# Kernel optimization log

Hardware: AMD Instinct MI355X
Metric: run time of the kernel (lower is better)

## Reference

```python
import jax, jax.numpy as jnp
import numpy as np
import math

N = 100000
E = 1600000
D_IN = 128
H = 128
OUT = 10
NEG = -1e30


def setup_inputs() -> dict:
    key = jax.random.key(0)
    ks = jax.random.split(key, 24)
    def lin(k, fi, fo):
        s = 1.0 / np.sqrt(fi)
        return jax.random.uniform(k, (fi, fo), jnp.float32, -s, s)
    inp = {
        'x': jax.random.normal(ks[0], (N, D_IN), jnp.float32),
        'edge_index': jax.random.randint(ks[1], (2, E), 0, N, jnp.int64),
        'W1': lin(ks[2], D_IN, H), 'b1': jnp.zeros((H,), jnp.float32),
        'ws1': lin(ks[3], H, 1), 'bs1': jnp.zeros((1,), jnp.float32),
        'W2': lin(ks[4], H, H), 'b2': jnp.zeros((H,), jnp.float32),
        'ws2': lin(ks[5], H, 1), 'bs2': jnp.zeros((1,), jnp.float32),
        'W3': lin(ks[6], H, H), 'b3': jnp.zeros((H,), jnp.float32),
        'ws3': lin(ks[7], H, 1), 'bs3': jnp.zeros((1,), jnp.float32),
        'M1': lin(ks[8], 2 * H, H), 'bm1': jnp.zeros((H,), jnp.float32),
        'M2': lin(ks[9], H, H // 2), 'bm2': jnp.zeros((H // 2,), jnp.float32),
        'M3': lin(ks[10], H // 2, OUT), 'bm3': jnp.zeros((OUT,), jnp.float32),
    }
    return inp


def _gcn(x, W, b, src, dst, node_mask, edge_mask):
    # GCNConv with self-loops: deg[i] = self_loop + in_degree over valid edges
    deg = node_mask + jax.ops.segment_sum(edge_mask, dst, num_segments=N)
    dinv = jnp.where(deg > 0, jax.lax.rsqrt(deg), 0.0)
    coef = edge_mask * dinv[src] * dinv[dst]            # [E]
    agg = jax.ops.segment_sum(coef[:, None] * x[src], dst, num_segments=N)
    agg = agg + (node_mask * dinv * dinv)[:, None] * x   # self-loop term
    return (agg @ W + b) * node_mask[:, None]


def _sag_pool(x, ws, bs, src, dst, node_mask, edge_mask, k):
    # score via 1-dim GCNConv, top-k (ratio 0.5) select, tanh gating, edge filtering
    score = _gcn(x, ws, bs, src, dst, node_mask, edge_mask)[:, 0]
    _, idx = jax.lax.top_k(jnp.where(node_mask > 0, score, -jnp.inf), k)
    new_mask = jnp.zeros((N,), x.dtype).at[idx].set(1.0)
    x_new = x * jnp.tanh(score)[:, None] * new_mask[:, None]
    e_new = edge_mask * new_mask[src] * new_mask[dst]
    return x_new, new_mask, e_new


def _readout(x, mask, k):
    mean = jnp.sum(x * mask[:, None], axis=0) / k
    mx = jnp.max(jnp.where(mask[:, None] > 0, x, NEG), axis=0)
    return jnp.concatenate([mean, mx])[None, :]   # [1, 2H]


def reference(x, edge_index, W1, b1, ws1, bs1, W2, b2, ws2, bs2, W3, b3, ws3, bs3, M1, bm1, M2, bm2, M3, bm3):
    src, dst = edge_index[0], edge_index[1]
    nm0 = jnp.ones((N,), jnp.float32)
    em0 = jnp.ones((E,), jnp.float32)
    k1 = math.ceil(0.5 * N)
    k2 = math.ceil(0.5 * k1)
    k3 = math.ceil(0.5 * k2)

    h1 = jax.nn.relu(_gcn(x, W1, b1, src, dst, nm0, em0))
    x1, nm1, em1 = _sag_pool(h1, ws1, bs1, src, dst, nm0, em0, k1)
    r1 = _readout(x1, nm1, k1)

    h2 = jax.nn.relu(_gcn(x1, W2, b2, src, dst, nm1, em1))
    x2, nm2, em2 = _sag_pool(h2, ws2, bs2, src, dst, nm1, em1, k2)
    r2 = _readout(x2, nm2, k2)

    h3 = jax.nn.relu(_gcn(x2, W3, b3, src, dst, nm2, em2))
    x3, nm3, em3 = _sag_pool(h3, ws3, bs3, src, dst, nm2, em2, k3)
    r3 = _readout(x3, nm3, k3)

    readout = r1 + r2 + r3                              # [1, 2H]
    y = jax.nn.relu(readout @ M1 + bm1)
    y = jax.nn.relu(y @ M2 + bm2)
    y = y @ M3 + bm3
    return jax.nn.log_softmax(y, axis=1)
```

## Files before the change

### kernel.cpp

```cpp
#include <hip/hip_runtime.h>
#include <cstdint>
#include <cstddef>

#define NN 100000
#define EE 1600000
#define HH 128
#define NB_N 391
#define NBKT 391
#define CAP 5120
#define NCH 16
#define SPC 25


typedef float f32x2 __attribute__((ext_vector_type(2)));
typedef float f32x4 __attribute__((ext_vector_type(4)));
typedef short bf16x8 __attribute__((ext_vector_type(8)));

static __device__ __forceinline__ unsigned fsort_(float f){
  unsigned u = __float_as_uint(f);
  return (u & 0x80000000u) ? ~u : (u | 0x80000000u);
}
static __device__ __forceinline__ unsigned bfbits_(float f){
  unsigned u = __float_as_uint(f);
  return (u + 0x7FFFu + ((u >> 16) & 1u)) >> 16;
}
static __device__ __forceinline__ unsigned bfpack_(float f0, float f1){
  return bfbits_(f0) | (bfbits_(f1) << 16);
}
static __device__ __forceinline__ float bflo_(unsigned u){ return __uint_as_float(u << 16); }
static __device__ __forceinline__ float bfhi_(unsigned u){ return __uint_as_float(u & 0xFFFF0000u); }

__global__ void k_init(const int* __restrict__ ei, unsigned* __restrict__ state,
                       unsigned* __restrict__ bktcnt,
                       const float* __restrict__ W0, const float* __restrict__ W1,
                       const float* __restrict__ W2,
                       unsigned short* __restrict__ WtH, unsigned short* __restrict__ WtL){
  int t = threadIdx.x;
  if(blockIdx.x == 3){
    if(t < 64){
      int v = ei[2*t + 1];
      unsigned long long m = __ballot(v != 0);
      if(t == 0) state[8] = (m == 0ull) ? 1u : 0u;
    }
    if(t >= 12 && t < 24) state[t] = 0u;
    for(int j=t; j<NBKT; j+=256) bktcnt[j] = 0u;
  } else {
    int m = blockIdx.x;
    const float* W = (m==0)?W0:((m==1)?W1:W2);
    unsigned short* th = WtH + m*16384;
    unsigned short* tl = WtL + m*16384;
    for(int i=t; i<16384; i+=256){
      int k = i & 127, n = i >> 7;
      float w = W[k*128 + n];
      unsigned hb = bfbits_(w);
      float hf = __uint_as_float(hb<<16);
      unsigned lb = bfbits_(w - hf);
      th[n*128 + k] = (unsigned short)hb;
      tl[n*128 + k] = (unsigned short)lb;
    }
  }
}

__global__ __launch_bounds__(256) void k_binA(const int* __restrict__ ei,
                     const unsigned* __restrict__ state,
                     unsigned* __restrict__ bktcnt, unsigned* __restrict__ staging){
  __shared__ unsigned lcnt[NBKT];
  __shared__ unsigned gbase[NBKT];
  __shared__ unsigned lloc[NBKT];
  __shared__ unsigned pfx[512];
  __shared__ unsigned sortv[4096];
  __shared__ unsigned short bktid[4096];
  int t = threadIdx.x;
  for(int j=t; j<NBKT; j+=256){ lcnt[j] = 0u; lloc[j] = 0u; }
  bool i64 = (state[8] != 0u);
  int e0 = blockIdx.x*4096;
  int es[16], ed[16];
  #pragma unroll
  for(int k=0;k<16;k++){
    int e = e0 + k*256 + t;
    int s = -1, d = 0;
    if(e < EE){
      if(i64){ s = ei[2*e]; d = ei[2*EE + 2*e]; }
      else   { s = ei[e];   d = ei[EE + e]; }
    }
    es[k] = s; ed[k] = d;
  }
  __syncthreads();
  #pragma unroll
  for(int k=0;k<16;k++){
    if(es[k] >= 0) atomicAdd(&lcnt[ed[k]>>8], 1u);
  }
  __syncthreads();
  int j0 = t, j1 = t + 256;
  pfx[j0] = (j0 < NBKT) ? lcnt[j0] : 0u;
  pfx[j1] = (j1 < NBKT) ? lcnt[j1] : 0u;
  __syncthreads();
  for(int off=1; off<512; off<<=1){
    unsigned u0 = (j0 >= off) ? pfx[j0-off] : 0u;
    unsigned u1 = (j1 >= off) ? pfx[j1-off] : 0u;
    __syncthreads();
    pfx[j0] += u0;
    pfx[j1] += u1;
    __syncthreads();
  }
  unsigned total = pfx[NBKT-1];
  for(int j=t; j<NBKT; j+=256){
    unsigned c = lcnt[j];
    gbase[j] = c ? atomicAdd(&bktcnt[j], c) : 0u;
  }
  __syncthreads();
  #pragma unroll
  for(int k=0;k<16;k++){
    if(es[k] >= 0){
      int b = ed[k] >> 8;
      unsigned slot = (pfx[b] - lcnt[b]) + atomicAdd(&lloc[b], 1u);
      sortv[slot] = (unsigned)es[k] | (((unsigned)(ed[k] & 255)) << 17);
      bktid[slot] = (unsigned short)b;
    }
  }
  __syncthreads();
  for(unsigned i=t; i<total; i+=256){
    unsigned b = bktid[i];
    unsigned local = i - (pfx[b] - lcnt[b]);
    unsigned off = gbase[b] + local;
    if(off < CAP) staging[b*CAP + off] = sortv[i];
  }
}

__global__ __launch_bounds__(256) void k_binB(const unsigned* __restrict__ staging,
                     const unsigned* __restrict__ bktcnt,
                     int* __restrict__ rs, int* __restrict__ rl, int* __restrict__ col,
                     float* __restrict__ dinv){
  __shared__ unsigned hist[256];
  __shared__ unsigned pref[256];
  __shared__ unsigned lfill[256];
  __shared__ unsigned baseSh;
  __shared__ int colsh[CAP];
  int t = threadIdx.x;
  int b = blockIdx.x;
  unsigned s = 0;
  for(int j=t; j<b; j+=256) s += bktcnt[j];
  pref[t] = s;
  __syncthreads();
  for(int off=128; off>0; off>>=1){
    if(t < off) pref[t] += pref[t+off];
    __syncthreads();
  }
  if(t == 0) baseSh = pref[0];
  __syncthreads();
  unsigned base = baseSh;
  unsigned cnt = bktcnt[b]; if(cnt > CAP) cnt = CAP;
  hist[t] = 0u; lfill[t] = 0u;
  __syncthreads();
  const unsigned* st = staging + (unsigned)b*CAP;
  for(unsigned i=t; i<cnt; i+=256) atomicAdd(&hist[st[i]>>17], 1u);
  __syncthreads();
  unsigned h = hist[t];
  pref[t] = h;
  __syncthreads();
  for(int off=1; off<256; off<<=1){
    unsigned u = (t >= off) ? pref[t-off] : 0u;
    __syncthreads();
    pref[t] += u;
    __syncthreads();
  }
  unsigned excl = pref[t] - h;
  int node = b*256 + t;
  if(node < NN){
    rs[node] = (int)(base + excl);
    rl[node] = (int)h;
    dinv[node] = rsqrtf(1.f + (float)h);
  }
  __syncthreads();
  pref[t] = excl;
  __syncthreads();
  for(unsigned i=t; i<cnt; i+=256){
    unsigned w = st[i];
    unsigned dl = w >> 17;
    unsigned pos = pref[dl] + atomicAdd(&lfill[dl], 1u);
    colsh[pos] = (int)(w & 0x1FFFFu);
  }
  __syncthreads();
  for(unsigned i=t; i<cnt; i+=256) col[base+i] = colsh[i];
}

template<int MODE>
__global__ __launch_bounds__(256) void k_gemmM(const void* __restrict__ xin_,
        const float* __restrict__ gate, const float* __restrict__ dinv,
        const int* __restrict__ alist, int nrows,
        const unsigned short* __restrict__ WtH, const unsigned short* __restrict__ WtL,
        unsigned short* __restrict__ y16){
  __shared__ __attribute__((aligned(16))) unsigned short sWh[128*128];
  __shared__ __attribute__((aligned(16))) unsigned short sWl[128*128];
  __shared__ __attribute__((aligned(16))) unsigned short sB[4][16*128];
  int t = threadIdx.x;
  for(int f = t; f < 2048; f += 256){
    int colw = f >> 4, kc = f & 15;
    uint4 vh = *(const uint4*)(WtH + colw*128 + kc*8);
    uint4 vl = *(const uint4*)(WtL + colw*128 + kc*8);
    int dst = colw*128 + ((kc ^ (colw & 15)) << 3);
    *(uint4*)&sWh[dst] = vh;
    *(uint4*)&sWl[dst] = vl;
  }
  int lane = t & 63, wid = t >> 6;
  int lg = lane >> 4, lc = lane & 15;
  int rb = blockIdx.x*64 + wid*16;
  int arow = rb + lc;
  int anode = 0;
  if(arow < nrows) anode = MODE ? alist[arow] : arow;
  bf16x8 a_h[4], a_l[4];
  if(MODE){
    const unsigned short* xp = (const unsigned short*)xin_ + (size_t)anode*HH + lg*8;
    #pragma unroll
    for(int kw=0;kw<4;kw++) a_h[kw] = *(const bf16x8*)(xp + kw*32);
  } else {
    const float* xp = (const float*)xin_ + (size_t)anode*HH + lg*8;
    #pragma unroll
    for(int kw=0;kw<4;kw++){
      float4 x0 = *(const float4*)(xp + kw*32);
      float4 x1 = *(const float4*)(xp + kw*32 + 4);
      float xs[8] = {x0.x,x0.y,x0.z,x0.w,x1.x,x1.y,x1.z,x1.w};
      #pragma unroll
      for(int e=0;e<8;e++){
        unsigned hb = bfbits_(xs[e]);
        float hf = __uint_as_float(hb<<16);
        unsigned lb = bfbits_(xs[e]-hf);
        a_h[kw][e] = (short)hb;
        a_l[kw][e] = (short)lb;
      }
    }
  }
  __syncthreads();
  f32x4 acc[8];
  #pragma unroll
  for(int c=0;c<8;c++) acc[c] = (f32x4){0.f,0.f,0.f,0.f};
  #pragma unroll
  for(int kw=0;kw<4;kw++){
    int kch = kw*4 + lg;
    bf16x8 bh[8], bl[8];
    #pragma unroll
    for(int c=0;c<8;c++){
      int idx = (c*16 + lc)*128 + ((kch ^ lc) << 3);
      bh[c] = *(const bf16x8*)&sWh[idx];
      bl[c] = *(const bf16x8*)&sWl[idx];
    }
    #pragma unroll
    for(int c=0;c<8;c++)
      acc[c] = __builtin_amdgcn_mfma_f32_16x16x32_bf16(a_h[kw], bh[c], acc[c], 0,0,0);
    if(MODE){
      #pragma unroll
      for(int c=0;c<8;c++)
        acc[c] = __builtin_amdgcn_mfma_f32_16x16x32_bf16(a_h[kw], bl[c], acc[c], 0,0,0);
    } else {
      #pragma unroll
      for(int c=0;c<8;c++)
        acc[c] = __builtin_amdgcn_mfma_f32_16x16x32_bf16(a_l[kw], bh[c], acc[c], 0,0,0);
      #pragma unroll
      for(int c=0;c<8;c++)
        acc[c] = __builtin_amdgcn_mfma_f32_16x16x32_bf16(a_h[kw], bl[c], acc[c], 0,0,0);
    }
  }
  float s[4];
  #pragma unroll
  for(int r=0;r<4;r++){
    int gr = rb + lg*4 + r;
    float sv = 0.f;
    if(gr < nrows){
      int nd = MODE ? alist[gr] : gr;
      sv = MODE ? dinv[nd]*gate[nd] : dinv[nd];
    }
    s[r] = sv;
  }
  #pragma unroll
  for(int c=0;c<8;c++){
    #pragma unroll
    for(int r=0;r<4;r++)
      sB[wid][(lg*4+r)*128 + c*16 + lc] = (unsigned short)bfbits_(acc[c][r]*s[r]);
  }
  #pragma unroll
  for(int it=0; it<4; it++){
    int row = it*4 + lg;
    int grow = rb + row;
    uint4 v = *(const uint4*)&sB[wid][row*128 + lc*8];
    if(grow < nrows){
      int nd = MODE ? alist[grow] : grow;
      *(uint4*)&y16[(size_t)nd*HH + lc*8] = v;
    }
  }
}

#define ACCQ(V) do{ \
  f32x2 t0,t1,t2,t3; \
  t0.x=__uint_as_float((V).x<<16); t0.y=__uint_as_float((V).x&0xFFFF0000u); \
  t1.x=__uint_as_float((V).y<<16); t1.y=__uint_as_float((V).y&0xFFFF0000u); \
  t2.x=__uint_as_float((V).z<<16); t2.y=__uint_as_float((V).z&0xFFFF0000u); \
  t3.x=__uint_as_float((V).w<<16); t3.y=__uint_as_float((V).w&0xFFFF0000u); \
  a01+=t0; a23+=t1; a45+=t2; a67+=t3; }while(0)

template<int LIST>
__global__ __launch_bounds__(256) void k_agg(const unsigned short* __restrict__ y16,
        const float* __restrict__ dinv,
        const int* __restrict__ rs, const int* __restrict__ rl,
        const int* __restrict__ col, const int* __restrict__ alist,
        const float* __restrict__ bias, const float* __restrict__ wsc,
        unsigned short* __restrict__ h16, float* __restrict__ p,
        unsigned* __restrict__ hist){
  if(blockIdx.x < 512) hist[blockIdx.x*256 + threadIdx.x] = 0u;
  int w = (blockIdx.x*256 + threadIdx.x) >> 6;
  int lane = threadIdx.x & 63;
  int g = lane >> 4, c = lane & 15;
  int node = LIST ? alist[w] : w;
  float di = dinv[node];
  int e0 = rs[node], len = rl[node];
  const char* yb = (const char*)y16;
  unsigned lc16 = (unsigned)(c << 4);
  int chunk = (len + 3) >> 2;
  int ib = g*chunk;
  int ie = ib + chunk; if(ie > len) ie = len;
  f32x2 a01 = {0.f,0.f}, a23 = {0.f,0.f}, a45 = {0.f,0.f}, a67 = {0.f,0.f};
  const int* ce = col + e0;
  int i = ib;
  for(; i+3 < ie; i += 4){
    int c0 = ce[i], c1 = ce[i+1], c2 = ce[i+2], c3 = ce[i+3];
    uint4 v0 = *(const uint4*)(yb + (((unsigned)c0<<8) | lc16));
    uint4 v1 = *(const uint4*)(yb + (((unsigned)c1<<8) | lc16));
    uint4 v2 = *(const uint4*)(yb + (((unsigned)c2<<8) | lc16));
    uint4 v3 = *(const uint4*)(yb + (((unsigned)c3<<8) | lc16));
    ACCQ(v0); ACCQ(v1); ACCQ(v2); ACCQ(v3);
  }
  for(; i < ie; i++){
    int c0 = ce[i];
    uint4 v0 = *(const uint4*)(yb + (((unsigned)c0<<8) | lc16));
    ACCQ(v0);
  }
  float a0=a01.x, a1=a01.y, a2=a23.x, a3=a23.y, a4=a45.x, a5=a45.y, a6=a67.x, a7=a67.y;
  a0 += __shfl_xor(a0,16,64); a0 += __shfl_xor(a0,32,64);
  a1 += __shfl_xor(a1,16,64); a1 += __shfl_xor(a1,32,64);
  a2 += __shfl_xor(a2,16,64); a2 += __shfl_xor(a2,32,64);
  a3 += __shfl_xor(a3,16,64); a3 += __shfl_xor(a3,32,64);
  a4 += __shfl_xor(a4,16,64); a4 += __shfl_xor(a4,32,64);
  a5 += __shfl_xor(a5,16,64); a5 += __shfl_xor(a5,32,64);
  a6 += __shfl_xor(a6,16,64); a6 += __shfl_xor(a6,32,64);
  a7 += __shfl_xor(a7,16,64); a7 += __shfl_xor(a7,32,64);
  uint4 sv = *(const uint4*)(yb + (((unsigned)node<<8) | lc16));
  const float4* b4 = (const float4*)bias;
  float4 bb0 = b4[2*c], bb1 = b4[2*c+1];
  float o0 = fmaxf(fmaf(di, a0 + bflo_(sv.x), bb0.x), 0.f);
  float o1 = fmaxf(fmaf(di, a1 + bfhi_(sv.x), bb0.y), 0.f);
  float o2 = fmaxf(fmaf(di, a2 + bflo_(sv.y), bb0.z), 0.f);
  float o3 = fmaxf(fmaf(di, a3 + bfhi_(sv.y), bb0.w), 0.f);
  float o4 = fmaxf(fmaf(di, a4 + bflo_(sv.z), bb1.x), 0.f);
  float o5 = fmaxf(fmaf(di, a5 + bfhi_(sv.z), bb1.y), 0.f);
  float o6 = fmaxf(fmaf(di, a6 + bflo_(sv.w), bb1.z), 0.f);
  float o7 = fmaxf(fmaf(di, a7 + bfhi_(sv.w), bb1.w), 0.f);
  if(g == 0){
    uint4 o;
    o.x = bfpack_(o0,o1); o.y = bfpack_(o2,o3);
    o.z = bfpack_(o4,o5); o.w = bfpack_(o6,o7);
    ((uint4*)(h16 + (size_t)node*HH))[c] = o;
  }
  const float4* w4 = (const float4*)wsc;
  float4 w0 = w4[2*c], w1 = w4[2*c+1];
  float pp = o0*w0.x + o1*w0.y + o2*w0.z + o3*w0.w
           + o4*w1.x + o5*w1.y + o6*w1.z + o7*w1.w;
  pp += __shfl_xor(pp, 1, 64);
  pp += __shfl_xor(pp, 2, 64);
  pp += __shfl_xor(pp, 4, 64);
  pp += __shfl_xor(pp, 8, 64);
  if(lane == 0) p[node] = di*pp;
}

template<int LIST>
__global__ void k_score(const float* __restrict__ p, const float* __restrict__ dinv,
                        const int* __restrict__ rs, const int* __restrict__ rl,
                        const int* __restrict__ col, const int* __restrict__ alist, int n,
                        const float* __restrict__ bs, float* __restrict__ score,
                        unsigned* __restrict__ key, unsigned* __restrict__ hist){
  int w = blockIdx.x*256 + threadIdx.x;
  if(w >= n) return;
  int i = LIST ? alist[w] : w;
  float di = dinv[i];
  float s = 0.f;
  int e0 = rs[i], len = rl[i];
  const int* ce = col + e0;
  int e = 0;
  for(; e+3 < len; e += 4){
    int c0 = ce[e], c1 = ce[e+1], c2 = ce[e+2], c3 = ce[e+3];
    s += (p[c0] + p[c1]) + (p[c2] + p[c3]);
  }
  for(; e < len; e++) s += p[ce[e]];
  float sc = di*(s + p[i]) + bs[0];
  score[i] = sc;
  unsigned kv = fsort_(sc);
  key[i] = kv;
  atomicAdd(&hist[kv>>16], 1u);
}

__global__ void k_hist_lo(const unsigned* __restrict__ key, const unsigned* __restrict__ state,
                          unsigned* __restrict__ histB){
  int i = blockIdx.x*256 + threadIdx.x;
  if(i < NN){
    unsigned kv = key[i];
    if((kv >> 16) == state[0]) atomicAdd(&histB[kv & 0xFFFFu], 1u);
  }
}
__global__ void k_pick(const unsigned* __restrict__ hist, unsigned* __restrict__ state,
                       int k_in, int mode){
  __shared__ unsigned csum[256];
  __shared__ unsigned vrow[256];
  __shared__ int rowSh;
  __shared__ unsigned aboveSh;
  int t = threadIdx.x;
  const uint4* h4 = (const uint4*)(hist + t*256);
  unsigned s = 0;
  for(int j=0;j<64;j++){ uint4 v = h4[j]; s += v.x+v.y+v.z+v.w; }
  csum[t] = s;
  if(t == 0) rowSh = -1;
  __syncthreads();
  for(int off=1; off<256; off<<=1){
    unsigned v = (t+off < 256) ? csum[t+off] : 0u;
    __syncthreads();
    csum[t] += v;
    __syncthreads();
  }
  unsigned k = (mode == 0) ? (unsigned)k_in : state[1];
  unsigned above = csum[t] - s;
  if(above < k && above + s >= k){ rowSh = t; aboveSh = above; }
  __syncthreads();
  int row = rowSh;
  if(row >= 0){
    vrow[t] = hist[row*256 + t];
    __syncthreads();
    for(int off=1; off<256; off<<=1){
      unsigned u = (t+off < 256) ? vrow[t+off] : 0u;
      __syncthreads();
      vrow[t] += u;
      __syncthreads();
    }
    unsigned above2 = aboveSh;
    unsigned sincl = vrow[t];
    unsigned snext = (t < 255) ? vrow[t+1] : 0u;
    bool cond  = (above2 + sincl >= k);
    bool condn = (above2 + snext >= k);
    if(cond && !condn){
      unsigned run = above2 + snext;
      if(mode == 0){ state[0] = (unsigned)(row*256+t); state[1] = k - run; }
      else { state[2] = (state[0] << 16) | (unsigned)(row*256+t); state[3] = k - run; }
    }
  }
}

__global__ __launch_bounds__(256) void k_maskCR(unsigned* __restrict__ key,
        const float* __restrict__ score, const unsigned* __restrict__ state,
        const unsigned short* __restrict__ h16,
        unsigned* __restrict__ selb, float* __restrict__ gate,
        int* __restrict__ alist_out, unsigned* __restrict__ acounter,
        float* __restrict__ rpart, int slotbase){
  __shared__ int wcnt[4];
  __shared__ int priorSh;
  __shared__ int redi[256];
  __shared__ float gl[256];
  __shared__ unsigned char slf[256];
  __shared__ float4 red[256];
  __shared__ float out2[256];
  int t = threadIdx.x;
  int i = blockIdx.x*256 + t;
  unsigned T = state[2];
  int trem = (int)state[3];
  unsigned kv = (i < NN) ? key[i] : 0u;
  bool match = (kv == T);
  unsigned long long m = __ballot(match);
  int lane = t & 63, wid = t >> 6;
  if(lane == 0) wcnt[wid] = __popcll(m);
  if(t == 0) priorSh = 0;
  __syncthreads();
  int hasMatch = wcnt[0] | wcnt[1] | wcnt[2] | wcnt[3];
  int bbase = blockIdx.x*256;
  if(hasMatch){
    int cm = 0;
    for(int j = t*4; j < bbase; j += 1024){
      uint4 kk = *(const uint4*)&key[j];
      cm += (kk.x==T) + (kk.y==T) + (kk.z==T) + (kk.w==T);
    }
    redi[t] = cm;
    __syncthreads();
    for(int off=128; off>0; off>>=1){
      if(t < off) redi[t] += redi[t+off];
      __syncthreads();
    }
    if(t == 0) priorSh = redi[0];
    __syncthreads();
  }
  int pre = 0;
  for(int w=0; w<wid; w++) pre += wcnt[w];
  int lrank = __popcll(m & ((1ull << lane) - 1ull));
  int rank = priorSh + pre + lrank;
  bool sel = (kv > T) || (match && rank < trem);
  float gg = sel ? tanhf(score[i]) : 0.f;
  gl[t] = gg;
  slf[t] = sel ? 1 : 0;
  if(i < NN){
    gate[i] = gg;
    if(!sel) key[i] = 0u;
  }
  unsigned long long sm = __ballot(sel);
  if(lane == 0){
    int widx = blockIdx.x*4 + wid;
    selb[widx*2]   = (unsigned)sm;
    selb[widx*2+1] = (unsigned)(sm >> 32);
  }
  unsigned abase = 0;
  if(lane == 0) abase = atomicAdd(acounter, (unsigned)__popcll(sm));
  abase = (unsigned)__shfl((int)abase, 0, 64);
  if(sel) alist_out[abase + __popcll(sm & ((1ull << lane) - 1ull))] = i;
  __syncthreads();
  int ch = t & 15;
  int slot = t >> 4;
  float mm[8] = {0,0,0,0,0,0,0,0};
  float MM[8] = {-1e30f,-1e30f,-1e30f,-1e30f,-1e30f,-1e30f,-1e30f,-1e30f};
  for(int itr=0; itr<16; itr++){
    int nl = slot + itr*16;
    int node = bbase + nl;
    if(node < NN && slf[nl]){
      float g = gl[nl];
      uint4 v = ((const uint4*)(h16 + (size_t)node*HH))[ch];
      float x0 = g*bflo_(v.x), x1 = g*bfhi_(v.x);
      float x2 = g*bflo_(v.y), x3 = g*bfhi_(v.y);
      float x4 = g*bflo_(v.z), x5 = g*bfhi_(v.z);
      float x6 = g*bflo_(v.w), x7 = g*bfhi_(v.w);
      mm[0]+=x0; mm[1]+=x1; mm[2]+=x2; mm[3]+=x3;
      mm[4]+=x4; mm[5]+=x5; mm[6]+=x6; mm[7]+=x7;
      MM[0]=fmaxf(MM[0],x0); MM[1]=fmaxf(MM[1],x1); MM[2]=fmaxf(MM[2],x2); MM[3]=fmaxf(MM[3],x3);
      MM[4]=fmaxf(MM[4],x4); MM[5]=fmaxf(MM[5],x5); MM[6]=fmaxf(MM[6],x6); MM[7]=fmaxf(MM[7],x7);
    }
  }
  #pragma unroll
  for(int half=0; half<2; half++){
    red[t] = make_float4(mm[half*4+0],mm[half*4+1],mm[half*4+2],mm[half*4+3]);
    __syncthreads();
    if(t < 16){
      float4 sacc = red[t];
      for(int j=1;j<16;j++){
        float4 o = red[t + 16*j];
        sacc.x += o.x; sacc.y += o.y; sacc.z += o.z; sacc.w += o.w;
      }
      int d = t*8 + half*4;
      out2[d+0] = sacc.x; out2[d+1] = sacc.y; out2[d+2] = sacc.z; out2[d+3] = sacc.w;
    }
    __syncthreads();
    red[t] = make_float4(MM[half*4+0],MM[half*4+1],MM[half*4+2],MM[half*4+3]);
    __syncthreads();
    if(t < 16){
      float4 sacc = red[t];
      for(int j=1;j<16;j++){
        float4 o = red[t + 16*j];
        sacc.x = fmaxf(sacc.x,o.x); sacc.y = fmaxf(sacc.y,o.y);
        sacc.z = fmaxf(sacc.z,o.z); sacc.w = fmaxf(sacc.w,o.w);
      }
      int d = 128 + t*8 + half*4;
      out2[d+0] = sacc.x; out2[d+1] = sacc.y; out2[d+2] = sacc.z; out2[d+3] = sacc.w;
    }
    __syncthreads();
  }
  rpart[(size_t)(slotbase + blockIdx.x)*256 + t] = out2[t];
}

__global__ __launch_bounds__(256) void k_compact(const int* __restrict__ alist, int n,
        const unsigned* __restrict__ selb,
        const int* __restrict__ rs_old, const int* __restrict__ rl_old,
        const int* __restrict__ col_old,
        int* __restrict__ rs_new, int* __restrict__ rl_new, int* __restrict__ col_new,
        float* __restrict__ dinv, unsigned* __restrict__ ecnt){
  __shared__ unsigned gcnt[16];
  __shared__ unsigned gbase[16];
  __shared__ unsigned blkbase;
  int t = threadIdx.x;
  int g = t >> 4, lane = t & 15;
  int gsh = ((t >> 4) & 3) * 16;
  int idx = blockIdx.x*16 + g;
  int node = -1, e0 = 0, len = 0;
  if(idx < n){ node = alist[idx]; e0 = rs_old[node]; len = rl_old[node]; }
  int cnt = 0;
  for(int i=lane; i<len; i+=16){
    int s = col_old[e0+i];
    cnt += (int)((selb[s>>5] >> (s&31)) & 1u);
  }
  cnt += __shfl_xor(cnt,1,64); cnt += __shfl_xor(cnt,2,64);
  cnt += __shfl_xor(cnt,4,64); cnt += __shfl_xor(cnt,8,64);
  if(lane == 0) gcnt[g] = (node >= 0) ? (unsigned)cnt : 0u;
  __syncthreads();
  if(t == 0){
    unsigned s = 0;
    for(int j=0;j<16;j++){ gbase[j] = s; s += gcnt[j]; }
    blkbase = s ? atomicAdd(ecnt, s) : 0u;
  }
  __syncthreads();
  unsigned base = blkbase + gbase[g];
  if(node >= 0 && lane == 0){
    rs_new[node] = (int)base;
    rl_new[node] = cnt;
    dinv[node] = rsqrtf(1.f + (float)cnt);
  }
  int pos = (int)base;
  for(int i0=0; i0<len; i0+=16){
    int i = i0 + lane;
    bool keep = false; int s = 0;
    if(i < len){ s = col_old[e0+i]; keep = ((selb[s>>5] >> (s&31)) & 1u) != 0u; }
    unsigned long long b = __ballot(keep);
    unsigned gb = (unsigned)((b >> gsh) & 0xFFFFull);
    int rank = __popc(gb & ((1u << lane) - 1u));
    if(keep) col_new[pos + rank] = s;
    pos += __popc(gb);
  }
}

__global__ void k_red(const float* __restrict__ rpart, float* __restrict__ rpart2){
  int l = blockIdx.x >> 4, c = blockIdx.x & 15;
  int t = threadIdx.x;
  int j0 = c*SPC, j1 = j0 + SPC; if(j1 > NB_N) j1 = NB_N;
  const float* rp = rpart + (size_t)l*NB_N*256;
  float r;
  if(t < 128){
    float s0=0.f,s1=0.f,s2=0.f,s3=0.f;
    int j = j0;
    for(; j+3 < j1; j += 4){
      s0 += rp[(size_t)(j  )*256 + t];
      s1 += rp[(size_t)(j+1)*256 + t];
      s2 += rp[(size_t)(j+2)*256 + t];
      s3 += rp[(size_t)(j+3)*256 + t];
    }
    for(; j < j1; j++) s0 += rp[(size_t)j*256 + t];
    r = (s0+s1)+(s2+s3);
  } else {
    float m0=-1e30f,m1=-1e30f,m2=-1e30f,m3=-1e30f;
    int j = j0;
    for(; j+3 < j1; j += 4){
      m0 = fmaxf(m0, rp[(size_t)(j  )*256 + t]);
      m1 = fmaxf(m1, rp[(size_t)(j+1)*256 + t]);
      m2 = fmaxf(m2, rp[(size_t)(j+2)*256 + t]);
      m3 = fmaxf(m3, rp[(size_t)(j+3)*256 + t]);
    }
    for(; j < j1; j++) m0 = fmaxf(m0, rp[(size_t)j*256 + t]);
    r = fmaxf(fmaxf(m0,m1), fmaxf(m2,m3));
  }
  rpart2[(size_t)blockIdx.x*256 + t] = r;
}

__global__ void k_mlp(const float* __restrict__ rpart2,
                      const float* __restrict__ M1, const float* __restrict__ bm1,
                      const float* __restrict__ M2, const float* __restrict__ bm2,
                      const float* __restrict__ M3, const float* __restrict__ bm3,
                      float* __restrict__ out){
  __shared__ float R[256];
  __shared__ float y1[128];
  __shared__ float y2[64];
  __shared__ float y3[16];
  int t = threadIdx.x;
  const float kinv[3] = {1.f/50000.f, 1.f/25000.f, 1.f/12500.f};
  if(t < 128){
    float acc = 0.f;
    for(int l=0; l<3; l++){
      float s = 0.f;
      #pragma unroll
      for(int c=0; c<NCH; c++) s += rpart2[(size_t)(l*NCH+c)*256 + t];
      acc += s * kinv[l];
    }
    R[t] = acc;
  } else {
    float acc = 0.f;
    for(int l=0; l<3; l++){
      float m = -1e30f;
      #pragma unroll
      for(int c=0; c<NCH; c++) m = fmaxf(m, rpart2[(size_t)(l*NCH+c)*256 + t]);
      acc += m;
    }
    R[t] = acc;
  }
  __syncthreads();
  if(t < 128){
    float a = bm1[t];
    for(int d=0; d<256; d++) a += R[d]*M1[d*128+t];
    y1[t] = fmaxf(a, 0.f);
  }
  __syncthreads();
  if(t < 64){
    float a = bm2[t];
    for(int d=0; d<128; d++) a += y1[d]*M2[d*64+t];
    y2[t] = fmaxf(a, 0.f);
  }
  __syncthreads();
  if(t < 10){
    float a = bm3[t];
    for(int d=0; d<64; d++) a += y2[d]*M3[d*10+t];
    y3[t] = a;
  }
  __syncthreads();
  if(t == 0){
    float mx = -1e30f;
    for(int o=0;o<10;o++) mx = fmaxf(mx, y3[o]);
    float s = 0.f;
    for(int o=0;o<10;o++) s += expf(y3[o]-mx);
    float ls = logf(s);
    for(int o=0;o<10;o++) out[o] = y3[o] - mx - ls;
  }
}

extern "C" void kernel_launch(void* const* d_in, const int* in_sizes, int n_in,
                              void* d_out, int out_size, void* d_ws, size_t ws_size,
                              hipStream_t stream){
  (void)in_sizes; (void)n_in; (void)out_size; (void)ws_size;
  const float* x  = (const float*)d_in[0];
  const int*   ei = (const int*)d_in[1];
  const float* W[3]   = {(const float*)d_in[2],  (const float*)d_in[6],  (const float*)d_in[10]};
  const float* bb[3]  = {(const float*)d_in[3],  (const float*)d_in[7],  (const float*)d_in[11]};
  const float* wsc[3] = {(const float*)d_in[4],  (const float*)d_in[8],  (const float*)d_in[12]};
  const float* bsc[3] = {(const float*)d_in[5],  (const float*)d_in[9],  (const float*)d_in[13]};
  const float* M1  = (const float*)d_in[14];
  const float* bm1 = (const float*)d_in[15];
  const float* M2  = (const float*)d_in[16];
  const float* bm2 = (const float*)d_in[17];
  const float* M3  = (const float*)d_in[18];
  const float* bm3 = (const float*)d_in[19];
  float* out = (float*)d_out;

  char* base = (char*)d_ws;
  size_t off = 0;
  auto alloc = [&](size_t bytes)->char*{
    char* ptr = base + off;
    off += (bytes + 511) & ~(size_t)511;
    return ptr;
  };
  unsigned short* y16  = (unsigned short*)alloc((size_t)NN*HH*2);
  unsigned short* h16  = (unsigned short*)alloc((size_t)NN*HH*2);
  int*      col0      = (int*)     alloc((size_t)EE*4);
  int*      col1      = (int*)     alloc((size_t)EE*4);
  int*      col2      = (int*)     alloc((size_t)EE*4);
  unsigned* staging   = (unsigned*)alloc((size_t)NBKT*CAP*4);
  int*      rs0       = (int*)     alloc((size_t)NN*4);
  int*      rl0       = (int*)     alloc((size_t)NN*4);
  int*      rs1       = (int*)     alloc((size_t)NN*4);
  int*      rl1       = (int*)     alloc((size_t)NN*4);
  int*      rs2       = (int*)     alloc((size_t)NN*4);
  int*      rl2       = (int*)     alloc((size_t)NN*4);
  float*    dinv      = (float*)   alloc((size_t)NN*4);
  float*    pbuf      = (float*)   alloc((size_t)NN*4);
  float*    score     = (float*)   alloc((size_t)NN*4);
  float*    gate      = (float*)   alloc((size_t)NN*4);
  unsigned* key       = (unsigned*)alloc((size_t)NN*4);
  unsigned* selb      = (unsigned*)alloc((size_t)3200*4);
  int*      alistA    = (int*)     alloc((size_t)50000*4);
  int*      alistB    = (int*)     alloc((size_t)25000*4);
  unsigned* hist      = (unsigned*)alloc((size_t)2*65536*4);
  unsigned* bktcnt    = (unsigned*)alloc((size_t)(NBKT+1)*4);
  unsigned* state     = (unsigned*)alloc(256);
  float*    rpart     = (float*)   alloc((size_t)3*NB_N*256*4);
  float*    rpart2    = (float*)   alloc((size_t)3*NCH*256*4);
  unsigned short* WtH = (unsigned short*)alloc((size_t)3*16384*2);
  unsigned short* WtL = (unsigned short*)alloc((size_t)3*16384*2);

  k_init<<<4,256,0,stream>>>(ei, state, bktcnt, W[0], W[1], W[2], WtH, WtL);
  k_binA<<<NBKT,256,0,stream>>>(ei, state, bktcnt, staging);
  k_binB<<<NBKT,256,0,stream>>>(staging, bktcnt, rs0, rl0, col0, dinv);

  k_gemmM<0><<<1563,256,0,stream>>>(x, nullptr, dinv, nullptr, NN, WtH, WtL, y16);
  k_agg<0><<<25000,256,0,stream>>>(y16, dinv, rs0, rl0, col0, nullptr, bb[0], wsc[0], h16, pbuf, hist);
  k_score<0><<<NB_N,256,0,stream>>>(pbuf, dinv, rs0, rl0, col0, nullptr, NN, bsc[0], score, key, hist);
  k_pick<<<1,256,0,stream>>>(hist, state, 50000, 0);
  k_hist_lo<<<NB_N,256,0,stream>>>(key, state, hist + 65536);
  k_pick<<<1,256,0,stream>>>(hist + 65536, state, 0, 1);
  k_maskCR<<<NB_N,256,0,stream>>>(key, score, state, h16, selb, gate, alistA, state+12, rpart, 0);
  k_compact<<<3125,256,0,stream>>>(alistA, 50000, selb, rs0, rl0, col0, rs1, rl1, col1, dinv, state+16);

  k_gemmM<1><<<782,256,0,stream>>>(h16, gate, dinv, alistA, 50000, WtH+16384, WtL+16384, y16);
  k_agg<1><<<12500,256,0,stream>>>(y16, dinv, rs1, rl1, col1, alistA, bb[1], wsc[1], h16, pbuf, hist);
  k_score<1><<<196,256,0,stream>>>(pbuf, dinv, rs1, rl1, col1, alistA, 50000, bsc[1], score, key, hist);
  k_pick<<<1,256,0,stream>>>(hist, state, 25000, 0);
  k_hist_lo<<<NB_N,256,0,stream>>>(key, state, hist + 65536);
  k_pick<<<1,256,0,stream>>>(hist + 65536, state, 0, 1);
  k_maskCR<<<NB_N,256,0,stream>>>(key, score, state, h16, selb, gate, alistB, state+13, rpart, NB_N);
  k_compact<<<1563,256,0,stream>>>(alistB, 25000, selb, rs1, rl1, col1, rs2, rl2, col2, dinv, state+17);

  k_gemmM<1><<<391,256,0,stream>>>(h16, gate, dinv, alistB, 25000, WtH+2*16384, WtL+2*16384, y16);
  k_agg<1><<<6250,256,0,stream>>>(y16, dinv, rs2, rl2, col2, alistB, bb[2], wsc[2], h16, pbuf, hist);
  k_score<1><<<98,256,0,stream>>>(pbuf, dinv, rs2, rl2, col2, alistB, 25000, bsc[2], score, key, hist);
  k_pick<<<1,256,0,stream>>>(hist, state, 12500, 0);
  k_hist_lo<<<NB_N,256,0,stream>>>(key, state, hist + 65536);
  k_pick<<<1,256,0,stream>>>(hist + 65536, state, 0, 1);
  k_maskCR<<<NB_N,256,0,stream>>>(key, score, state, h16, selb, gate, alistA, state+14, rpart, 2*NB_N);

  k_red<<<3*NCH,256,0,stream>>>(rpart, rpart2);
  k_mlp<<<1,256,0,stream>>>(rpart2, M1, bm1, M2, bm2, M3, bm3, out);
}
```

Measured before the change: 643.6 us.

## Fuse top-k selection chain and final reduction into cooperative kernels

Merges the score, histogram pick, low-bits histogram, second pick and mask/readout kernels of each pooling level into one cooperative kernel that uses grid syncs in place of separate launches. The reduction and MLP kernels are likewise fused into one cooperative kernel. The goal is to remove about a dozen small launches and their gaps, many of which were single-block picks. In exchange, each stage now pays grid-wide barriers and threadfences, and the score stage runs on 391 blocks even at later levels where fewer nodes remain, so some blocks sit idle.

New measurement: 1.839 ms. 2.86x slower.

```diff
diff --git a/kernel.cpp b/kernel.cpp
--- a/kernel.cpp
+++ b/kernel.cpp
@@ -1,6 +1,9 @@
 #include <hip/hip_runtime.h>
+#include <hip/hip_cooperative_groups.h>
 #include <cstdint>
 #include <cstddef>
+
+namespace cg = cooperative_groups;
 
 #define NN 100000
 #define EE 1600000
@@ -370,42 +373,8 @@
   if(lane == 0) p[node] = di*pp;
 }
 
-template<int LIST>
-__global__ void k_score(const float* __restrict__ p, const float* __restrict__ dinv,
-                        const int* __restrict__ rs, const int* __restrict__ rl,
-                        const int* __restrict__ col, const int* __restrict__ alist, int n,
-                        const float* __restrict__ bs, float* __restrict__ score,
-                        unsigned* __restrict__ key, unsigned* __restrict__ hist){
-  int w = blockIdx.x*256 + threadIdx.x;
-  if(w >= n) return;
-  int i = LIST ? alist[w] : w;
-  float di = dinv[i];
-  float s = 0.f;
-  int e0 = rs[i], len = rl[i];
-  const int* ce = col + e0;
-  int e = 0;
-  for(; e+3 < len; e += 4){
-    int c0 = ce[e], c1 = ce[e+1], c2 = ce[e+2], c3 = ce[e+3];
-    s += (p[c0] + p[c1]) + (p[c2] + p[c3]);
-  }
-  for(; e < len; e++) s += p[ce[e]];
-  float sc = di*(s + p[i]) + bs[0];
-  score[i] = sc;
-  unsigned kv = fsort_(sc);
-  key[i] = kv;
-  atomicAdd(&hist[kv>>16], 1u);
-}
-
-__global__ void k_hist_lo(const unsigned* __restrict__ key, const unsigned* __restrict__ state,
-                          unsigned* __restrict__ histB){
-  int i = blockIdx.x*256 + threadIdx.x;
-  if(i < NN){
-    unsigned kv = key[i];
-    if((kv >> 16) == state[0]) atomicAdd(&histB[kv & 0xFFFFu], 1u);
-  }
-}
-__global__ void k_pick(const unsigned* __restrict__ hist, unsigned* __restrict__ state,
-                       int k_in, int mode){
+__device__ void pick_dev(const unsigned* __restrict__ hist, unsigned* __restrict__ state,
+                         int k_in, int mode){
   __shared__ unsigned csum[256];
   __shared__ unsigned vrow[256];
   __shared__ int rowSh;
@@ -450,7 +419,7 @@
   }
 }
 
-__global__ __launch_bounds__(256) void k_maskCR(unsigned* __restrict__ key,
+__device__ void mask_dev(unsigned* __restrict__ key,
         const float* __restrict__ score, const unsigned* __restrict__ state,
         const unsigned short* __restrict__ h16,
         unsigned* __restrict__ selb, float* __restrict__ gate,
@@ -565,6 +534,57 @@
   rpart[(size_t)(slotbase + blockIdx.x)*256 + t] = out2[t];
 }
 
+struct SelArgs {
+  const float* p; const float* dinv; const int* rs; const int* rl;
+  const int* col; const int* alist; int n;
+  const float* bs; float* score; unsigned* key;
+  unsigned* hist; unsigned* histB; unsigned* state; int kk;
+  const unsigned short* h16; unsigned* selb; float* gate;
+  int* alist_out; unsigned* acounter; float* rpart; int slotbase;
+};
+
+template<int LIST>
+__global__ __launch_bounds__(256) void k_select(SelArgs a){
+  cg::grid_group gg = cg::this_grid();
+  int t = threadIdx.x, b = blockIdx.x;
+  {
+    int w = b*256 + t;
+    if(w < a.n){
+      int i = LIST ? a.alist[w] : w;
+      float di = a.dinv[i];
+      float s = 0.f;
+      int e0 = a.rs[i], len = a.rl[i];
+      const int* ce = a.col + e0;
+      int e = 0;
+      for(; e+3 < len; e += 4){
+        int c0 = ce[e], c1 = ce[e+1], c2 = ce[e+2], c3 = ce[e+3];
+        s += (a.p[c0] + a.p[c1]) + (a.p[c2] + a.p[c3]);
+      }
+      for(; e < len; e++) s += a.p[ce[e]];
+      float sc = di*(s + a.p[i]) + a.bs[0];
+      a.score[i] = sc;
+      unsigned kv = fsort_(sc);
+      a.key[i] = kv;
+      atomicAdd(&a.hist[kv>>16], 1u);
+    }
+  }
+  __threadfence(); gg.sync(); __threadfence();
+  if(b == 0) pick_dev(a.hist, a.state, a.kk, 0);
+  __threadfence(); gg.sync(); __threadfence();
+  {
+    unsigned hi = a.state[0];
+    for(int i = b*256 + t; i < NN; i += gridDim.x*256){
+      unsigned kv = a.key[i];
+      if((kv >> 16) == hi) atomicAdd(&a.histB[kv & 0xFFFFu], 1u);
+    }
+  }
+  __threadfence(); gg.sync(); __threadfence();
+  if(b == 0) pick_dev(a.histB, a.state, 0, 1);
+  __threadfence(); gg.sync(); __threadfence();
+  mask_dev(a.key, a.score, a.state, a.h16, a.selb, a.gate, a.alist_out,
+           a.acounter, a.rpart, a.slotbase);
+}
+
 __global__ __launch_bounds__(256) void k_compact(const int* __restrict__ alist, int n,
         const unsigned* __restrict__ selb,
         const int* __restrict__ rs_old, const int* __restrict__ rl_old,
@@ -614,48 +634,50 @@
   }
 }
 
-__global__ void k_red(const float* __restrict__ rpart, float* __restrict__ rpart2){
-  int l = blockIdx.x >> 4, c = blockIdx.x & 15;
-  int t = threadIdx.x;
-  int j0 = c*SPC, j1 = j0 + SPC; if(j1 > NB_N) j1 = NB_N;
-  const float* rp = rpart + (size_t)l*NB_N*256;
-  float r;
-  if(t < 128){
-    float s0=0.f,s1=0.f,s2=0.f,s3=0.f;
-    int j = j0;
-    for(; j+3 < j1; j += 4){
-      s0 += rp[(size_t)(j  )*256 + t];
-      s1 += rp[(size_t)(j+1)*256 + t];
-      s2 += rp[(size_t)(j+2)*256 + t];
-      s3 += rp[(size_t)(j+3)*256 + t];
-    }
-    for(; j < j1; j++) s0 += rp[(size_t)j*256 + t];
-    r = (s0+s1)+(s2+s3);
-  } else {
-    float m0=-1e30f,m1=-1e30f,m2=-1e30f,m3=-1e30f;
-    int j = j0;
-    for(; j+3 < j1; j += 4){
-      m0 = fmaxf(m0, rp[(size_t)(j  )*256 + t]);
-      m1 = fmaxf(m1, rp[(size_t)(j+1)*256 + t]);
-      m2 = fmaxf(m2, rp[(size_t)(j+2)*256 + t]);
-      m3 = fmaxf(m3, rp[(size_t)(j+3)*256 + t]);
-    }
-    for(; j < j1; j++) m0 = fmaxf(m0, rp[(size_t)j*256 + t]);
-    r = fmaxf(fmaxf(m0,m1), fmaxf(m2,m3));
-  }
-  rpart2[(size_t)blockIdx.x*256 + t] = r;
-}
-
-__global__ void k_mlp(const float* __restrict__ rpart2,
+__global__ __launch_bounds__(256) void k_final(const float* __restrict__ rpart,
+                      float* __restrict__ rpart2,
                       const float* __restrict__ M1, const float* __restrict__ bm1,
                       const float* __restrict__ M2, const float* __restrict__ bm2,
                       const float* __restrict__ M3, const float* __restrict__ bm3,
                       float* __restrict__ out){
+  cg::grid_group gg = cg::this_grid();
+  int t = threadIdx.x;
+  {
+    int l = blockIdx.x >> 4, c = blockIdx.x & 15;
+    int j0 = c*SPC, j1 = j0 + SPC; if(j1 > NB_N) j1 = NB_N;
+    const float* rp = rpart + (size_t)l*NB_N*256;
+    float r;
+    if(t < 128){
+      float s0=0.f,s1=0.f,s2=0.f,s3=0.f;
+      int j = j0;
+      for(; j+3 < j1; j += 4){
+        s0 += rp[(size_t)(j  )*256 + t];
+        s1 += rp[(size_t)(j+1)*256 + t];
+        s2 += rp[(size_t)(j+2)*256 + t];
+        s3 += rp[(size_t)(j+3)*256 + t];
+      }
+      for(; j < j1; j++) s0 += rp[(size_t)j*256 + t];
+      r = (s0+s1)+(s2+s3);
+    } else {
+      float m0=-1e30f,m1=-1e30f,m2=-1e30f,m3=-1e30f;
+      int j = j0;
+      for(; j+3 < j1; j += 4){
+        m0 = fmaxf(m0, rp[(size_t)(j  )*256 + t]);
+        m1 = fmaxf(m1, rp[(size_t)(j+1)*256 + t]);
+        m2 = fmaxf(m2, rp[(size_t)(j+2)*256 + t]);
+        m3 = fmaxf(m3, rp[(size_t)(j+3)*256 + t]);
+      }
+      for(; j < j1; j++) m0 = fmaxf(m0, rp[(size_t)j*256 + t]);
+      r = fmaxf(fmaxf(m0,m1), fmaxf(m2,m3));
+    }
+    rpart2[(size_t)blockIdx.x*256 + t] = r;
+  }
+  __threadfence(); gg.sync(); __threadfence();
+  if(blockIdx.x != 0) return;
   __shared__ float R[256];
   __shared__ float y1[128];
   __shared__ float y2[64];
   __shared__ float y3[16];
-  int t = threadIdx.x;
   const float kinv[3] = {1.f/50000.f, 1.f/25000.f, 1.f/12500.f};
   if(t < 128){
     float acc = 0.f;
@@ -764,30 +786,40 @@
 
   k_gemmM<0><<<1563,256,0,stream>>>(x, nullptr, dinv, nullptr, NN, WtH, WtL, y16);
   k_agg<0><<<25000,256,0,stream>>>(y16, dinv, rs0, rl0, col0, nullptr, bb[0], wsc[0], h16, pbuf, hist);
-  k_score<0><<<NB_N,256,0,stream>>>(pbuf, dinv, rs0, rl0, col0, nullptr, NN, bsc[0], score, key, hist);
-  k_pick<<<1,256,0,stream>>>(hist, state, 50000, 0);
-  k_hist_lo<<<NB_N,256,0,stream>>>(key, state, hist + 65536);
-  k_pick<<<1,256,0,stream>>>(hist + 65536, state, 0, 1);
-  k_maskCR<<<NB_N,256,0,stream>>>(key, score, state, h16, selb, gate, alistA, state+12, rpart, 0);
+  {
+    SelArgs sa{pbuf, dinv, rs0, rl0, col0, nullptr, NN, bsc[0], score, key,
+               hist, hist+65536, state, 50000, h16, selb, gate, alistA, state+12, rpart, 0};
+    void* args[] = {&sa};
+    (void)hipLaunchCooperativeKernel((void*)k_select<0>, dim3(NB_N), dim3(256), args, 0, stream);
+  }
   k_compact<<<3125,256,0,stream>>>(alistA, 50000, selb, rs0, rl0, col0, rs1, rl1, col1, dinv, state+16);
 
   k_gemmM<1><<<782,256,0,stream>>>(h16, gate, dinv, alistA, 50000, WtH+16384, WtL+16384, y16);
   k_agg<1><<<12500,256,0,stream>>>(y16, dinv, rs1, rl1, col1, alistA, bb[1], wsc[1], h16, pbuf, hist);
-  k_score<1><<<196,256,0,stream>>>(pbuf, dinv, rs1, rl1, col1, alistA, 50000, bsc[1], score, key, hist);
-  k_pick<<<1,256,0,stream>>>(hist, state, 25000, 0);
-  k_hist_lo<<<NB_N,256,0,stream>>>(key, state, hist + 65536);
-  k_pick<<<1,256,0,stream>>>(hist + 65536, state, 0, 1);
-  k_maskCR<<<NB_N,256,0,stream>>>(key, score, state, h16, selb, gate, alistB, state+13, rpart, NB_N);
+  {
+    SelArgs sa{pbuf, dinv, rs1, rl1, col1, alistA, 50000, bsc[1], score, key,
+               hist, hist+65536, state, 25000, h16, selb, gate, alistB, state+13, rpart, NB_N};
+    void* args[] = {&sa};
+    (void)hipLaunchCooperativeKernel((void*)k_select<1>, dim3(NB_N), dim3(256), args, 0, stream);
+  }
   k_compact<<<1563,256,0,stream>>>(alistB, 25000, selb, rs1, rl1, col1, rs2, rl2, col2, dinv, state+17);
 
   k_gemmM<1><<<391,256,0,stream>>>(h16, gate, dinv, alistB, 25000, WtH+2*16384, WtL+2*16384, y16);
   k_agg<1><<<6250,256,0,stream>>>(y16, dinv, rs2, rl2, col2, alistB, bb[2], wsc[2], h16, pbuf, hist);
-  k_score<1><<<98,256,0,stream>>>(pbuf, dinv, rs2, rl2, col2, alistB, 25000, bsc[2], score, key, hist);
-  k_pick<<<1,256,0,stream>>>(hist, state, 12500, 0);
-  k_hist_lo<<<NB_N,256,0,stream>>>(key, state, hist + 65536);
-  k_pick<<<1,256,0,stream>>>(hist + 65536, state, 0, 1);
-  k_maskCR<<<NB_N,256,0,stream>>>(key, score, state, h16, selb, gate, alistA, state+14, rpart, 2*NB_N);
-
-  k_red<<<3*NCH,256,0,stream>>>(rpart, rpart2);
-  k_mlp<<<1,256,0,stream>>>(rpart2, M1, bm1, M2, bm2, M3, bm3, out);
-}
+  {
+    SelArgs sa{pbuf, dinv, rs2, rl2, col2, alistB, 25000, bsc[2], score, key,
+               hist, hist+65536, state, 12500, h16, selb, gate, alistA, state+14, rpart, 2*NB_N};
+    void* args[] = {&sa};
+    (void)hipLaunchCooperativeKernel((void*)k_select<1>, dim3(NB_N), dim3(256), args, 0, stream);
+  }
+
+  {
+    const float* rp = rpart; float* rp2 = rpart2;
+    const float* m1 = M1; const float* b1 = bm1;
+    const float* m2 = M2; const float* b2 = bm2;
+    const float* m3 = M3; const float* b3 = bm3;
+    float* op = out;
+    void* args[] = {&rp, &rp2, &m1, &b1, &m2, &b2, &m3, &b3, &op};
+    (void)hipLaunchCooperativeKernel((void*)k_final, dim3(3*NCH), dim3(256), args, 0, stream);
+  }
+}
```
